# Kernel tuning notes

Measured on AMD Instinct MI355X. Metric: run time of the kernel, lower is better.

## Reference

```python
import jax, jax.numpy as jnp
import numpy as np

LN_EPS = 1e-12  # BertLayerNorm default


def _digcn_forward(hidden_state, adjacency_matrix, Wl, bl, Ws, bs, Wr, br, ln_w, ln_b):
    B, S, D = hidden_state.shape
    temper = jnp.asarray(D, jnp.float32) ** 0.5
    i = jnp.arange(S)
    upper = (i[None, :] > i[:, None]).astype(hidden_state.dtype)  # strict upper: j > i
    lower = (i[None, :] < i[:, None]).astype(hidden_state.dtype)  # strict lower: j < i

    def layer(h, params):
        wl, b_l, ws, b_s, wr, b_r, g, beta = params
        # directed graph attention: softmax over full scores, then mask by adjacency and renormalize
        u = jnp.einsum('bid,bjd->bij', h, h) / temper            # [B,S,S]
        a = jax.nn.softmax(u, axis=-1)
        delta = a * adjacency_matrix
        attn = delta / (jnp.sum(delta, axis=-1, keepdims=True) + 1e-10)
        # three projections (torch Linear: x @ W.T + b)
        hl = h @ wl.T + b_l
        hs = h @ ws.T + b_s
        hr = h @ wr.T + b_r
        # split attention into strictly-upper (left), diagonal (self), strictly-lower (right)
        diag_a = jnp.diagonal(attn, axis1=1, axis2=2)            # [B,S]
        ctx = (jnp.einsum('bij,bjd->bid', attn * upper, hl)
               + diag_a[..., None] * hs
               + jnp.einsum('bij,bjd->bid', attn * lower, hr))
        # BertLayerNorm
        mean = ctx.mean(-1, keepdims=True)
        var = ctx.var(-1, keepdims=True)
        o = (ctx - mean) / jnp.sqrt(var + LN_EPS) * g + beta
        return jax.nn.relu(o), None

    out, _ = jax.lax.scan(layer, hidden_state, (Wl, bl, Ws, bs, Wr, br, ln_w, ln_b))
    return out


def setup_inputs() -> dict:
    key = jax.random.key(0)
    ks = jax.random.split(key, 6)
    B, S, D, L = 8, 1024, 768, 2
    scale = (1.0 / D) ** 0.5  # ~xavier scale for [D,D] linears
    hidden_state = jax.random.normal(ks[0], (B, S, D), jnp.float32)
    adjacency_matrix = (jax.random.uniform(ks[1], (B, S, S)) < 0.05).astype(jnp.float32)
    Wl = jax.random.normal(ks[2], (L, D, D), jnp.float32) * scale
    Ws = jax.random.normal(ks[3], (L, D, D), jnp.float32) * scale
    Wr = jax.random.normal(ks[4], (L, D, D), jnp.float32) * scale
    bl = jnp.zeros((L, D), jnp.float32)
    bs = jnp.zeros((L, D), jnp.float32)
    br = jnp.zeros((L, D), jnp.float32)
    ln_w = jnp.ones((L, D), jnp.float32)
    ln_b = jnp.zeros((L, D), jnp.float32)
    return dict(hidden_state=hidden_state, adjacency_matrix=adjacency_matrix,
                Wl=Wl, bl=bl, Ws=Ws, bs=bs, Wr=Wr, br=br, ln_w=ln_w, ln_b=ln_b)


def reference(hidden_state, adjacency_matrix, Wl, bl, Ws, bs, Wr, br, ln_w, ln_b):
    return _digcn_forward(hidden_state, adjacency_matrix, Wl, bl, Ws, bs, Wr, br, ln_w, ln_b)
```

## Files before the change

kernel.cpp:

```cpp
#include <hip/hip_runtime.h>
#include <hip/hip_bf16.h>


using bf16 = __hip_bfloat16;
typedef __attribute__((ext_vector_type(8))) short short8;
typedef __attribute__((ext_vector_type(4))) float f32x4;

#define B_ 8
#define S_ 1024
#define D_ 768
#define BS_ 8192
#define SS_ 1048576L
#define SD_ 786432L
#define DD_ 589824L

__device__ __forceinline__ void gload16(const void* g, void* l) {
  __builtin_amdgcn_global_load_lds((const __attribute__((address_space(1))) void*)g,
                                   (__attribute__((address_space(3))) void*)l, 16, 0, 0);
}

__device__ __forceinline__ f32x4 mfma16(short8 a, short8 b, f32x4 c) {
  return __builtin_amdgcn_mfma_f32_16x16x32_bf16(a, b, c, 0, 0, 0);
}

__device__ __forceinline__ float wave_sum(float v) {
  #pragma unroll
  for (int o = 32; o; o >>= 1) v += __shfl_xor(v, o);
  return v;
}
__device__ __forceinline__ float wave_max(float v) {
  #pragma unroll
  for (int o = 32; o; o >>= 1) v = fmaxf(v, __shfl_xor(v, o));
  return v;
}

__device__ __forceinline__ void stage_tile(const bf16* g, long ld, int kt, short* s,
                                           int w, int lane) {
  #pragma unroll
  for (int i = 0; i < 4; ++i) {
    int rt = w * 32 + i * 8 + (lane >> 3);
    int ch = lane & 7;
    const bf16* src = g + (long)rt * ld + (long)kt * 64 + ((ch ^ (rt & 7)) << 3);
    gload16((const void*)src, (void*)(s + (w * 32 + i * 8) * 64));
  }
}

__device__ __forceinline__ short8 read_frag(const short* s, int r0, int kk, int lane) {
  int r = r0 + (lane & 15);
  int c = (kk << 2) + (lane >> 4);
  return *(const short8*)((const char*)s + r * 128 + ((c ^ (r & 7)) << 4));
}

__device__ __forceinline__ void gemm_loop(const bf16* A, long lda, const bf16* Bm, long ldb,
                                          int kt0, int kt1, short* As, short* Bs,
                                          f32x4 acc[4][4], int w, int lane, int wm, int wn) {
  for (int kt = kt0; kt < kt1; ++kt) {
    __syncthreads();
    stage_tile(A, lda, kt, As, w, lane);
    stage_tile(Bm, ldb, kt, Bs, w, lane);
    __syncthreads();
    #pragma unroll
    for (int kk = 0; kk < 2; ++kk) {
      short8 af[4], bfr[4];
      #pragma unroll
      for (int m = 0; m < 4; ++m) af[m] = read_frag(As, wm * 64 + m * 16, kk, lane);
      #pragma unroll
      for (int n = 0; n < 4; ++n) bfr[n] = read_frag(Bs, wn * 64 + n * 16, kk, lane);
      #pragma unroll
      for (int m = 0; m < 4; ++m)
        #pragma unroll
        for (int n = 0; n < 4; ++n)
          acc[m][n] = mfma16(af[m], bfr[n], acc[m][n]);
    }
  }
}

__global__ __launch_bounds__(256) void k_scores(const bf16* __restrict__ hb,
                                                float* __restrict__ out, float scale) {
  __shared__ short As[128 * 64], Bs[128 * 64];
  int b = blockIdx.z;
  int tid = threadIdx.x, w = tid >> 6, lane = tid & 63, wm = w >> 1, wn = w & 1;
  const bf16* A = hb + (long)b * SD_ + (long)blockIdx.x * 128 * D_;
  const bf16* Bp = hb + (long)b * SD_ + (long)blockIdx.y * 128 * D_;
  f32x4 acc[4][4] = {};
  gemm_loop(A, D_, Bp, D_, 0, 12, As, Bs, acc, w, lane, wm, wn);
  float* C = out + (long)b * SS_;
  int row0 = blockIdx.x * 128 + wm * 64, col0 = blockIdx.y * 128 + wn * 64;
  #pragma unroll
  for (int m = 0; m < 4; ++m) {
    int r = row0 + m * 16 + ((lane >> 4) << 2);
    #pragma unroll
    for (int n = 0; n < 4; ++n) {
      int c = col0 + n * 16 + (lane & 15);
      #pragma unroll
      for (int j = 0; j < 4; ++j) C[(long)(r + j) * S_ + c] = acc[m][n][j] * scale;
    }
  }
}

__global__ __launch_bounds__(256) void k_proj(const bf16* __restrict__ hb,
                                              const bf16* __restrict__ Wb,
                                              const float* __restrict__ bl,
                                              const float* __restrict__ bs,
                                              const float* __restrict__ br,
                                              bf16* __restrict__ hlT,
                                              bf16* __restrict__ hsb,
                                              bf16* __restrict__ hrT) {
  __shared__ short As[128 * 64], Bs[128 * 64];
  int z = blockIdx.z;
  int tid = threadIdx.x, w = tid >> 6, lane = tid & 63, wm = w >> 1, wn = w & 1;
  const bf16* A = hb + (long)blockIdx.x * 128 * D_;
  const bf16* Bp = Wb + (long)z * DD_ + (long)blockIdx.y * 128 * D_;
  f32x4 acc[4][4] = {};
  gemm_loop(A, D_, Bp, D_, 0, 12, As, Bs, acc, w, lane, wm, wn);
  const float* bias = (z == 0) ? bl : (z == 1) ? bs : br;
  int row0 = blockIdx.x * 128 + wm * 64, col0 = blockIdx.y * 128 + wn * 64;
  if (z == 1) {
    #pragma unroll
    for (int m = 0; m < 4; ++m) {
      int r = row0 + m * 16 + ((lane >> 4) << 2);
      #pragma unroll
      for (int n = 0; n < 4; ++n) {
        int c = col0 + n * 16 + (lane & 15);
        float bv = bias[c];
        #pragma unroll
        for (int j = 0; j < 4; ++j)
          hsb[(long)(r + j) * D_ + c] = __float2bfloat16(acc[m][n][j] + bv);
      }
    }
  } else {
    bf16* outT = (z == 0) ? hlT : hrT;
    #pragma unroll
    for (int m = 0; m < 4; ++m) {
      int r = row0 + m * 16 + ((lane >> 4) << 2);
      #pragma unroll
      for (int n = 0; n < 4; ++n) {
        int c = col0 + n * 16 + (lane & 15);
        float bv = bias[c];
        #pragma unroll
        for (int j = 0; j < 4; ++j)
          outT[(long)c * BS_ + r + j] = __float2bfloat16(acc[m][n][j] + bv);
      }
    }
  }
}

__global__ __launch_bounds__(256) void k_softmax(const float* __restrict__ scores,
                                                 const float* __restrict__ adj,
                                                 bf16* __restrict__ attnU,
                                                 bf16* __restrict__ attnL,
                                                 float* __restrict__ diag) {
  int wv = threadIdx.x >> 6, lane = threadIdx.x & 63;
  int row = blockIdx.x * 4 + wv;
  int i = row & (S_ - 1);
  const float* srow = scores + (long)row * S_;
  const float* arow = adj + (long)row * S_;
  float s[16], a[16], p[16];
  #pragma unroll
  for (int k = 0; k < 16; ++k) { int idx = k * 64 + lane; s[k] = srow[idx]; a[k] = arow[idx]; }
  float mx = -1e30f;
  #pragma unroll
  for (int k = 0; k < 16; ++k) mx = fmaxf(mx, s[k]);
  mx = wave_max(mx);
  float Z = 0.f, Sm = 0.f;
  #pragma unroll
  for (int k = 0; k < 16; ++k) { p[k] = __expf(s[k] - mx); Z += p[k]; Sm += p[k] * a[k]; }
  Z = wave_sum(Z); Sm = wave_sum(Sm);
  float inv = 1.0f / (Sm + 1e-10f * Z);
  #pragma unroll
  for (int k = 0; k < 16; ++k) {
    int j = k * 64 + lane;
    float at = p[k] * a[k] * inv;
    attnU[(long)row * S_ + j] = __float2bfloat16(j > i ? at : 0.f);
    attnL[(long)row * S_ + j] = __float2bfloat16(j < i ? at : 0.f);
    if (j == i) diag[row] = at;
  }
}

__global__ __launch_bounds__(256) void k_ctx(const bf16* __restrict__ attnU,
                                             const bf16* __restrict__ attnL,
                                             const bf16* __restrict__ hlT,
                                             const bf16* __restrict__ hrT,
                                             const bf16* __restrict__ hsb,
                                             const float* __restrict__ diag,
                                             float* __restrict__ ctx) {
  __shared__ short As[128 * 64], Bs[128 * 64];
  int b = blockIdx.z;
  int tid = threadIdx.x, w = tid >> 6, lane = tid & 63, wm = w >> 1, wn = w & 1;
  int rm = blockIdx.x * 128;
  int t = rm >> 6;
  const bf16* A1 = attnU + (long)b * SS_ + (long)rm * S_;
  const bf16* B1 = hlT + (long)blockIdx.y * 128 * BS_ + (long)b * S_;
  const bf16* A2 = attnL + (long)b * SS_ + (long)rm * S_;
  const bf16* B2 = hrT + (long)blockIdx.y * 128 * BS_ + (long)b * S_;
  f32x4 acc[4][4] = {};
  gemm_loop(A1, S_, B1, BS_, t, 16, As, Bs, acc, w, lane, wm, wn);
  gemm_loop(A2, S_, B2, BS_, 0, t + 2, As, Bs, acc, w, lane, wm, wn);
  int row0 = rm + wm * 64, col0 = blockIdx.y * 128 + wn * 64;
  #pragma unroll
  for (int m = 0; m < 4; ++m) {
    int r = row0 + m * 16 + ((lane >> 4) << 2);
    float dg[4];
    #pragma unroll
    for (int j = 0; j < 4; ++j) dg[j] = diag[b * S_ + r + j];
    #pragma unroll
    for (int n = 0; n < 4; ++n) {
      int c = col0 + n * 16 + (lane & 15);
      #pragma unroll
      for (int j = 0; j < 4; ++j) {
        long gr = (long)(b * S_ + r + j);
        float hv = __bfloat162float(hsb[gr * D_ + c]);
        ctx[gr * D_ + c] = acc[m][n][j] + dg[j] * hv;
      }
    }
  }
}

__global__ __launch_bounds__(256) void k_ln(const float* __restrict__ ctx,
                                            const float* __restrict__ g,
                                            const float* __restrict__ beta,
                                            float* __restrict__ outF,
                                            bf16* __restrict__ outB) {
  int wv = threadIdx.x >> 6, lane = threadIdx.x & 63;
  long row = (long)blockIdx.x * 4 + wv;
  const float* x = ctx + row * D_;
  float v[12]; float s = 0.f;
  #pragma unroll
  for (int k = 0; k < 12; ++k) { v[k] = x[k * 64 + lane]; s += v[k]; }
  s = wave_sum(s);
  float mean = s * (1.0f / 768.0f);
  float q = 0.f;
  #pragma unroll
  for (int k = 0; k < 12; ++k) { float d = v[k] - mean; q += d * d; }
  q = wave_sum(q);
  float inv = rsqrtf(fmaxf(q * (1.0f / 768.0f), 0.f) + 1e-12f);
  #pragma unroll
  for (int k = 0; k < 12; ++k) {
    int c = k * 64 + lane;
    float o = fmaxf((v[k] - mean) * inv * g[c] + beta[c], 0.f);
    if (outF) outF[row * D_ + c] = o;
    if (outB) outB[row * D_ + c] = __float2bfloat16(o);
  }
}

__global__ __launch_bounds__(256) void k_castf(const float* __restrict__ in,
                                               bf16* __restrict__ out) {
  long idx = ((long)blockIdx.x * 256 + threadIdx.x) * 4;
  float4 f = *(const float4*)(in + idx);
  out[idx] = __float2bfloat16(f.x);
  out[idx + 1] = __float2bfloat16(f.y);
  out[idx + 2] = __float2bfloat16(f.z);
  out[idx + 3] = __float2bfloat16(f.w);
}

__global__ __launch_bounds__(256) void k_castw(const float* __restrict__ wl,
                                               const float* __restrict__ ws_,
                                               const float* __restrict__ wr,
                                               bf16* __restrict__ out) {
  const float* src = (blockIdx.y == 0) ? wl : (blockIdx.y == 1) ? ws_ : wr;
  bf16* o = out + (long)blockIdx.y * DD_;
  long idx = ((long)blockIdx.x * 256 + threadIdx.x) * 4;
  float4 f = *(const float4*)(src + idx);
  o[idx] = __float2bfloat16(f.x);
  o[idx + 1] = __float2bfloat16(f.y);
  o[idx + 2] = __float2bfloat16(f.z);
  o[idx + 3] = __float2bfloat16(f.w);
}

extern "C" void kernel_launch(void* const* d_in, const int* in_sizes, int n_in,
                              void* d_out, int out_size, void* d_ws, size_t ws_size,
                              hipStream_t stream) {
  const float* hidden = (const float*)d_in[0];
  const float* adj    = (const float*)d_in[1];
  const float* Wl     = (const float*)d_in[2];
  const float* bl     = (const float*)d_in[3];
  const float* Ws     = (const float*)d_in[4];
  const float* bs     = (const float*)d_in[5];
  const float* Wr     = (const float*)d_in[6];
  const float* br     = (const float*)d_in[7];
  const float* lnw    = (const float*)d_in[8];
  const float* lnb    = (const float*)d_in[9];
  float* out = (float*)d_out;

  char* ws = (char*)d_ws;
  bf16*  hb    = (bf16*)(ws);
  bf16*  hlT   = (bf16*)(ws + 12582912);
  bf16*  hrT   = (bf16*)(ws + 25165824);
  bf16*  hsb   = (bf16*)(ws + 37748736);
  bf16*  Wb    = (bf16*)(ws + 50331648);
  float* diag  = (float*)(ws + 53870592);
  bf16*  attnU = (bf16*)(ws + 53903360);
  bf16*  attnL = (bf16*)(ws + 70680576);
  float* scores = (float*)(ws + 87457792);
  float* ctx = scores;

  const float scale = 0.03608439182435161f;

  k_castf<<<6144, 256, 0, stream>>>(hidden, hb);
  for (int l = 0; l < 2; ++l) {
    long wo = (long)l * DD_;
    k_castw<<<dim3(576, 3), 256, 0, stream>>>(Wl + wo, Ws + wo, Wr + wo, Wb);
    k_scores<<<dim3(8, 8, B_), 256, 0, stream>>>(hb, scores, scale);
    k_softmax<<<2048, 256, 0, stream>>>(scores, adj, attnU, attnL, diag);
    k_proj<<<dim3(64, 6, 3), 256, 0, stream>>>(hb, Wb, bl + l * D_, bs + l * D_,
                                               br + l * D_, hlT, hsb, hrT);
    k_ctx<<<dim3(8, 6, B_), 256, 0, stream>>>(attnU, attnL, hlT, hrT, hsb, diag, ctx);
    k_ln<<<2048, 256, 0, stream>>>(ctx, lnw + l * D_, lnb + l * D_,
                                   (l == 1) ? out : nullptr,
                                   (l == 1) ? (bf16*)nullptr : hb);
  }
}
```

Before: 379.0 us.

## Fuse masked softmax into score GEMM epilogue, defer normalization, double-buffer GEMMs

Drops the separate softmax kernel and the fp32 score buffer. The score GEMM epilogue now computes exp(score) without max subtraction, applies the adjacency mask, writes unnormalized upper and lower bf16 tiles plus the diagonal, and accumulates per-row sums Z and Sm with atomics into a buffer zeroed by a memset. The context GEMM applies 1/(Sm+1e-10·Z) in its epilogue. All GEMM loops gain LDS double buffering with prefetch of the next K tile, and weight casting for both layers is hoisted into a single launch. Without the max subtraction, exp can overflow if scores grow large, and the atomics make the row sums order-nondeterministic.

```diff
diff --git a/kernel.cpp b/kernel.cpp
--- a/kernel.cpp
+++ b/kernel.cpp
@@ -28,11 +28,6 @@
   for (int o = 32; o; o >>= 1) v += __shfl_xor(v, o);
   return v;
 }
-__device__ __forceinline__ float wave_max(float v) {
-  #pragma unroll
-  for (int o = 32; o; o >>= 1) v = fmaxf(v, __shfl_xor(v, o));
-  return v;
-}
 
 __device__ __forceinline__ void stage_tile(const bf16* g, long ld, int kt, short* s,
                                            int w, int lane) {
@@ -51,49 +46,88 @@
   return *(const short8*)((const char*)s + r * 128 + ((c ^ (r & 7)) << 4));
 }
 
-__device__ __forceinline__ void gemm_loop(const bf16* A, long lda, const bf16* Bm, long ldb,
-                                          int kt0, int kt1, short* As, short* Bs,
-                                          f32x4 acc[4][4], int w, int lane, int wm, int wn) {
+__device__ __forceinline__ void compute_tile(const short* As, const short* Bs,
+                                             f32x4 acc[4][4], int lane, int wm, int wn) {
+  #pragma unroll
+  for (int kk = 0; kk < 2; ++kk) {
+    short8 af[4], bfr[4];
+    #pragma unroll
+    for (int m = 0; m < 4; ++m) af[m] = read_frag(As, wm * 64 + m * 16, kk, lane);
+    #pragma unroll
+    for (int n = 0; n < 4; ++n) bfr[n] = read_frag(Bs, wn * 64 + n * 16, kk, lane);
+    #pragma unroll
+    for (int m = 0; m < 4; ++m)
+      #pragma unroll
+      for (int n = 0; n < 4; ++n)
+        acc[m][n] = mfma16(af[m], bfr[n], acc[m][n]);
+  }
+}
+
+__device__ __forceinline__ void gemm_db(const bf16* A, long lda, const bf16* Bm, long ldb,
+                                        int kt0, int kt1, short (*L)[8192],
+                                        f32x4 acc[4][4], int w, int lane, int wm, int wn) {
+  stage_tile(A, lda, kt0, L[0], w, lane);
+  stage_tile(Bm, ldb, kt0, L[1], w, lane);
+  asm volatile("s_waitcnt vmcnt(0)");
+  __syncthreads();
+  int cur = 0;
   for (int kt = kt0; kt < kt1; ++kt) {
+    if (kt + 1 < kt1) {
+      stage_tile(A, lda, kt + 1, L[2 * (cur ^ 1)], w, lane);
+      stage_tile(Bm, ldb, kt + 1, L[2 * (cur ^ 1) + 1], w, lane);
+    }
+    compute_tile(L[2 * cur], L[2 * cur + 1], acc, lane, wm, wn);
+    asm volatile("s_waitcnt vmcnt(0)");
     __syncthreads();
-    stage_tile(A, lda, kt, As, w, lane);
-    stage_tile(Bm, ldb, kt, Bs, w, lane);
-    __syncthreads();
-    #pragma unroll
-    for (int kk = 0; kk < 2; ++kk) {
-      short8 af[4], bfr[4];
-      #pragma unroll
-      for (int m = 0; m < 4; ++m) af[m] = read_frag(As, wm * 64 + m * 16, kk, lane);
-      #pragma unroll
-      for (int n = 0; n < 4; ++n) bfr[n] = read_frag(Bs, wn * 64 + n * 16, kk, lane);
-      #pragma unroll
-      for (int m = 0; m < 4; ++m)
-        #pragma unroll
-        for (int n = 0; n < 4; ++n)
-          acc[m][n] = mfma16(af[m], bfr[n], acc[m][n]);
-    }
+    cur ^= 1;
   }
 }
 
 __global__ __launch_bounds__(256) void k_scores(const bf16* __restrict__ hb,
-                                                float* __restrict__ out, float scale) {
-  __shared__ short As[128 * 64], Bs[128 * 64];
+                                                const float* __restrict__ adj,
+                                                bf16* __restrict__ paU,
+                                                bf16* __restrict__ paL,
+                                                float* __restrict__ diagpa,
+                                                float* __restrict__ Sm,
+                                                float* __restrict__ Zs,
+                                                float scale) {
+  __shared__ short L[4][8192];
   int b = blockIdx.z;
   int tid = threadIdx.x, w = tid >> 6, lane = tid & 63, wm = w >> 1, wn = w & 1;
   const bf16* A = hb + (long)b * SD_ + (long)blockIdx.x * 128 * D_;
   const bf16* Bp = hb + (long)b * SD_ + (long)blockIdx.y * 128 * D_;
   f32x4 acc[4][4] = {};
-  gemm_loop(A, D_, Bp, D_, 0, 12, As, Bs, acc, w, lane, wm, wn);
-  float* C = out + (long)b * SS_;
+  gemm_db(A, D_, Bp, D_, 0, 12, L, acc, w, lane, wm, wn);
   int row0 = blockIdx.x * 128 + wm * 64, col0 = blockIdx.y * 128 + wn * 64;
   #pragma unroll
   for (int m = 0; m < 4; ++m) {
-    int r = row0 + m * 16 + ((lane >> 4) << 2);
-    #pragma unroll
-    for (int n = 0; n < 4; ++n) {
-      int c = col0 + n * 16 + (lane & 15);
-      #pragma unroll
-      for (int j = 0; j < 4; ++j) C[(long)(r + j) * S_ + c] = acc[m][n][j] * scale;
+    int rbase = row0 + m * 16 + ((lane >> 4) << 2);
+    #pragma unroll
+    for (int j = 0; j < 4; ++j) {
+      int rs = rbase + j;
+      long rowg = (long)b * S_ + rs;
+      float psum = 0.f, pasum = 0.f;
+      #pragma unroll
+      for (int n = 0; n < 4; ++n) {
+        int cs = col0 + n * 16 + (lane & 15);
+        float p = __expf(acc[m][n][j] * scale);
+        float a = adj[rowg * S_ + cs];
+        bf16 pb = __float2bfloat16(p * a);
+        float pa = __bfloat162float(pb);
+        psum += p; pasum += pa;
+        paU[rowg * S_ + cs] = (cs > rs) ? pb : __float2bfloat16(0.f);
+        paL[rowg * S_ + cs] = (cs < rs) ? pb : __float2bfloat16(0.f);
+        if (cs == rs) diagpa[rowg] = pa;
+      }
+      #pragma unroll
+      for (int o = 1; o < 16; o <<= 1) {
+        psum += __shfl_xor(psum, o);
+        pasum += __shfl_xor(pasum, o);
+      }
+      if ((lane & 15) == 0) {
+        atomicAdd(&Sm[rowg], pasum);
+        atomicAdd(&Zs[rowg], psum);
+      }
     }
   }
 }
@@ -106,13 +140,13 @@
                                               bf16* __restrict__ hlT,
                                               bf16* __restrict__ hsb,
                                               bf16* __restrict__ hrT) {
-  __shared__ short As[128 * 64], Bs[128 * 64];
+  __shared__ short L[4][8192];
   int z = blockIdx.z;
   int tid = threadIdx.x, w = tid >> 6, lane = tid & 63, wm = w >> 1, wn = w & 1;
   const bf16* A = hb + (long)blockIdx.x * 128 * D_;
-  const bf16* Bp = Wb + (long)z * DD_ + (long)blockIdx.y * 128 * D_;
+  const bf16* Bp = Wb + (long)z * 2 * DD_ + (long)blockIdx.y * 128 * D_;
   f32x4 acc[4][4] = {};
-  gemm_loop(A, D_, Bp, D_, 0, 12, As, Bs, acc, w, lane, wm, wn);
+  gemm_db(A, D_, Bp, D_, 0, 12, L, acc, w, lane, wm, wn);
   const float* bias = (z == 0) ? bl : (z == 1) ? bs : br;
   int row0 = blockIdx.x * 128 + wm * 64, col0 = blockIdx.y * 128 + wn * 64;
   if (z == 1) {
@@ -145,72 +179,70 @@
   }
 }
 
-__global__ __launch_bounds__(256) void k_softmax(const float* __restrict__ scores,
-                                                 const float* __restrict__ adj,
-                                                 bf16* __restrict__ attnU,
-                                                 bf16* __restrict__ attnL,
-                                                 float* __restrict__ diag) {
-  int wv = threadIdx.x >> 6, lane = threadIdx.x & 63;
-  int row = blockIdx.x * 4 + wv;
-  int i = row & (S_ - 1);
-  const float* srow = scores + (long)row * S_;
-  const float* arow = adj + (long)row * S_;
-  float s[16], a[16], p[16];
-  #pragma unroll
-  for (int k = 0; k < 16; ++k) { int idx = k * 64 + lane; s[k] = srow[idx]; a[k] = arow[idx]; }
-  float mx = -1e30f;
-  #pragma unroll
-  for (int k = 0; k < 16; ++k) mx = fmaxf(mx, s[k]);
-  mx = wave_max(mx);
-  float Z = 0.f, Sm = 0.f;
-  #pragma unroll
-  for (int k = 0; k < 16; ++k) { p[k] = __expf(s[k] - mx); Z += p[k]; Sm += p[k] * a[k]; }
-  Z = wave_sum(Z); Sm = wave_sum(Sm);
-  float inv = 1.0f / (Sm + 1e-10f * Z);
-  #pragma unroll
-  for (int k = 0; k < 16; ++k) {
-    int j = k * 64 + lane;
-    float at = p[k] * a[k] * inv;
-    attnU[(long)row * S_ + j] = __float2bfloat16(j > i ? at : 0.f);
-    attnL[(long)row * S_ + j] = __float2bfloat16(j < i ? at : 0.f);
-    if (j == i) diag[row] = at;
-  }
-}
-
-__global__ __launch_bounds__(256) void k_ctx(const bf16* __restrict__ attnU,
-                                             const bf16* __restrict__ attnL,
+__global__ __launch_bounds__(256) void k_ctx(const bf16* __restrict__ paU,
+                                             const bf16* __restrict__ paL,
                                              const bf16* __restrict__ hlT,
                                              const bf16* __restrict__ hrT,
                                              const bf16* __restrict__ hsb,
-                                             const float* __restrict__ diag,
+                                             const float* __restrict__ diagpa,
+                                             const float* __restrict__ Sm,
+                                             const float* __restrict__ Zs,
                                              float* __restrict__ ctx) {
-  __shared__ short As[128 * 64], Bs[128 * 64];
+  __shared__ short L[4][8192];
   int b = blockIdx.z;
   int tid = threadIdx.x, w = tid >> 6, lane = tid & 63, wm = w >> 1, wn = w & 1;
   int rm = blockIdx.x * 128;
   int t = rm >> 6;
-  const bf16* A1 = attnU + (long)b * SS_ + (long)rm * S_;
+  const bf16* A1 = paU + (long)b * SS_ + (long)rm * S_;
   const bf16* B1 = hlT + (long)blockIdx.y * 128 * BS_ + (long)b * S_;
-  const bf16* A2 = attnL + (long)b * SS_ + (long)rm * S_;
+  const bf16* A2 = paL + (long)b * SS_ + (long)rm * S_;
   const bf16* B2 = hrT + (long)blockIdx.y * 128 * BS_ + (long)b * S_;
+  int ntU = 16 - t;
+  int nt = ntU + t + 2;
   f32x4 acc[4][4] = {};
-  gemm_loop(A1, S_, B1, BS_, t, 16, As, Bs, acc, w, lane, wm, wn);
-  gemm_loop(A2, S_, B2, BS_, 0, t + 2, As, Bs, acc, w, lane, wm, wn);
+
+  const bf16 *Ap, *Bp; int kt;
+  {
+    Ap = A1; Bp = B1; kt = t;
+    stage_tile(Ap, S_, kt, L[0], w, lane);
+    stage_tile(Bp, BS_, kt, L[1], w, lane);
+  }
+  asm volatile("s_waitcnt vmcnt(0)");
+  __syncthreads();
+  int cur = 0;
+  for (int q = 0; q < nt; ++q) {
+    if (q + 1 < nt) {
+      int qn = q + 1;
+      if (qn < ntU) { Ap = A1; Bp = B1; kt = t + qn; }
+      else          { Ap = A2; Bp = B2; kt = qn - ntU; }
+      stage_tile(Ap, S_, kt, L[2 * (cur ^ 1)], w, lane);
+      stage_tile(Bp, BS_, kt, L[2 * (cur ^ 1) + 1], w, lane);
+    }
+    compute_tile(L[2 * cur], L[2 * cur + 1], acc, lane, wm, wn);
+    asm volatile("s_waitcnt vmcnt(0)");
+    __syncthreads();
+    cur ^= 1;
+  }
+
   int row0 = rm + wm * 64, col0 = blockIdx.y * 128 + wn * 64;
   #pragma unroll
   for (int m = 0; m < 4; ++m) {
     int r = row0 + m * 16 + ((lane >> 4) << 2);
-    float dg[4];
-    #pragma unroll
-    for (int j = 0; j < 4; ++j) dg[j] = diag[b * S_ + r + j];
+    float dg[4], inv[4];
+    #pragma unroll
+    for (int j = 0; j < 4; ++j) {
+      long gr = (long)b * S_ + r + j;
+      dg[j] = diagpa[gr];
+      inv[j] = 1.0f / (Sm[gr] + 1e-10f * Zs[gr]);
+    }
     #pragma unroll
     for (int n = 0; n < 4; ++n) {
       int c = col0 + n * 16 + (lane & 15);
       #pragma unroll
       for (int j = 0; j < 4; ++j) {
-        long gr = (long)(b * S_ + r + j);
+        long gr = (long)b * S_ + r + j;
         float hv = __bfloat162float(hsb[gr * D_ + c]);
-        ctx[gr * D_ + c] = acc[m][n][j] + dg[j] * hv;
+        ctx[gr * D_ + c] = (acc[m][n][j] + dg[j] * hv) * inv[j];
       }
     }
   }
@@ -258,7 +290,7 @@
                                                const float* __restrict__ wr,
                                                bf16* __restrict__ out) {
   const float* src = (blockIdx.y == 0) ? wl : (blockIdx.y == 1) ? ws_ : wr;
-  bf16* o = out + (long)blockIdx.y * DD_;
+  bf16* o = out + (long)blockIdx.y * 2 * DD_;
   long idx = ((long)blockIdx.x * 256 + threadIdx.x) * 4;
   float4 f = *(const float4*)(src + idx);
   o[idx] = __float2bfloat16(f.x);
@@ -283,28 +315,29 @@
   float* out = (float*)d_out;
 
   char* ws = (char*)d_ws;
-  bf16*  hb    = (bf16*)(ws);
-  bf16*  hlT   = (bf16*)(ws + 12582912);
-  bf16*  hrT   = (bf16*)(ws + 25165824);
-  bf16*  hsb   = (bf16*)(ws + 37748736);
-  bf16*  Wb    = (bf16*)(ws + 50331648);
-  float* diag  = (float*)(ws + 53870592);
-  bf16*  attnU = (bf16*)(ws + 53903360);
-  bf16*  attnL = (bf16*)(ws + 70680576);
-  float* scores = (float*)(ws + 87457792);
-  float* ctx = scores;
-
+  bf16*  hb     = (bf16*)(ws);
+  bf16*  hlT    = (bf16*)(ws + 12582912);
+  bf16*  hrT    = (bf16*)(ws + 25165824);
+  bf16*  hsb    = (bf16*)(ws + 37748736);
+  bf16*  Wb     = (bf16*)(ws + 50331648);
+  float* diagpa = (float*)(ws + 57409536);
+  float* SmZ    = (float*)(ws + 57442304);
+  bf16*  paU    = (bf16*)(ws + 57507840);
+  bf16*  paL    = (bf16*)(ws + 74285056);
+  float* ctx    = (float*)(ws + 91062272);
+
+  float* Sm = SmZ;
+  float* Zs = SmZ + BS_;
   const float scale = 0.03608439182435161f;
 
   k_castf<<<6144, 256, 0, stream>>>(hidden, hb);
+  k_castw<<<dim3(1152, 3), 256, 0, stream>>>(Wl, Ws, Wr, Wb);
   for (int l = 0; l < 2; ++l) {
-    long wo = (long)l * DD_;
-    k_castw<<<dim3(576, 3), 256, 0, stream>>>(Wl + wo, Ws + wo, Wr + wo, Wb);
-    k_scores<<<dim3(8, 8, B_), 256, 0, stream>>>(hb, scores, scale);
-    k_softmax<<<2048, 256, 0, stream>>>(scores, adj, attnU, attnL, diag);
-    k_proj<<<dim3(64, 6, 3), 256, 0, stream>>>(hb, Wb, bl + l * D_, bs + l * D_,
-                                               br + l * D_, hlT, hsb, hrT);
-    k_ctx<<<dim3(8, 6, B_), 256, 0, stream>>>(attnU, attnL, hlT, hrT, hsb, diag, ctx);
+    hipMemsetAsync(SmZ, 0, 2 * BS_ * sizeof(float), stream);
+    k_scores<<<dim3(8, 8, B_), 256, 0, stream>>>(hb, adj, paU, paL, diagpa, Sm, Zs, scale);
+    k_proj<<<dim3(64, 6, 3), 256, 0, stream>>>(hb, Wb + (long)l * DD_, bl + l * D_,
+                                               bs + l * D_, br + l * D_, hlT, hsb, hrT);
+    k_ctx<<<dim3(8, 6, B_), 256, 0, stream>>>(paU, paL, hlT, hrT, hsb, diagpa, Sm, Zs, ctx);
     k_ln<<<2048, 256, 0, stream>>>(ctx, lnw + l * D_, lnb + l * D_,
                                    (l == 1) ? out : nullptr,
                                    (l == 1) ? (bf16*)nullptr : hb);
```

Result: faster. 351.5 us (-7.3%).
